# Kernel optimization log

Hardware: AMD Instinct MI355X
Metric: run time of the kernel (lower is better)

The kernel has to match this reference:

```python
import jax, jax.numpy as jnp
import numpy as np

NS, NR, D, H, O = 50000, 100000, 128, 128, 2
ESR, ERR, ESS = 1000000, 1600000, 800000


def _sage(x_src, x_dst, src, dst, Wl, bl, Wr, num_dst):
    # PyG SAGEConv(aggr='mean'): lin_l(mean_{j in N(i)} x_j) + lin_r(x_i)
    s = jax.ops.segment_sum(x_src[src], dst, num_segments=num_dst)
    cnt = jax.ops.segment_sum(jnp.ones(dst.shape, x_src.dtype), dst, num_segments=num_dst)
    agg = s / jnp.maximum(cnt, 1.0)[:, None]
    return agg @ Wl + bl + x_dst @ Wr


def setup_inputs() -> dict:
    key = jax.random.key(0)
    ks = jax.random.split(key, 32)
    f = lambda i, shp: jax.random.normal(ks[i], shp, jnp.float32) * 0.05
    inp = {"x_subject": f(0, (NS, D)), "x_roi": f(1, (NR, D))}
    wnames = ["w1_sr_l", "w1_sr_r", "w1_rr_l", "w1_rr_r", "w1_ss_l", "w1_ss_r",
              "w2_sr_l", "w2_sr_r", "w2_rr_l", "w2_rr_r", "w2_ss_l", "w2_ss_r"]
    for i, n in enumerate(wnames):
        inp[n] = f(2 + i, (D if n[1] == '1' else H, H))
    for n in ["b1_sr", "b1_rr", "b1_ss", "b2_sr", "b2_rr", "b2_ss"]:
        inp[n] = jnp.zeros((H,), jnp.float32)
    inp["lin_w"] = f(14, (H, O))
    inp["lin_b"] = jnp.zeros((O,), jnp.float32)
    inp["ei_sr_src"] = jax.random.randint(ks[20], (ESR,), 0, NS, jnp.int32)
    inp["ei_sr_dst"] = jax.random.randint(ks[21], (ESR,), 0, NR, jnp.int32)
    inp["ei_rr_src"] = jax.random.randint(ks[22], (ERR,), 0, NR, jnp.int32)
    inp["ei_rr_dst"] = jax.random.randint(ks[23], (ERR,), 0, NR, jnp.int32)
    inp["ei_ss_src"] = jax.random.randint(ks[24], (ESS,), 0, NS, jnp.int32)
    inp["ei_ss_dst"] = jax.random.randint(ks[25], (ESS,), 0, NS, jnp.int32)
    return inp


def reference(x_subject, x_roi,
              w1_sr_l, b1_sr, w1_sr_r, w1_rr_l, b1_rr, w1_rr_r, w1_ss_l, b1_ss, w1_ss_r,
              w2_sr_l, b2_sr, w2_sr_r, w2_rr_l, b2_rr, w2_rr_r, w2_ss_l, b2_ss, w2_ss_r,
              lin_w, lin_b,
              ei_sr_src, ei_sr_dst, ei_rr_src, ei_rr_dst, ei_ss_src, ei_ss_dst):
    # layer 1: HeteroConv with aggr='mean' over per-edge-type outputs
    r1 = 0.5 * (_sage(x_subject, x_roi, ei_sr_src, ei_sr_dst, w1_sr_l, b1_sr, w1_sr_r, NR)
                + _sage(x_roi, x_roi, ei_rr_src, ei_rr_dst, w1_rr_l, b1_rr, w1_rr_r, NR))
    s1 = _sage(x_subject, x_subject, ei_ss_src, ei_ss_dst, w1_ss_l, b1_ss, w1_ss_r, NS)
    r1, s1 = jax.nn.relu(r1), jax.nn.relu(s1)
    # layer 2 (roi branch is dead code w.r.t. the output, which reads only 'subject')
    s2 = _sage(s1, s1, ei_ss_src, ei_ss_dst, w2_ss_l, b2_ss, w2_ss_r, NS)
    s2 = jax.nn.relu(s2)
    return s2 @ lin_w + lin_b
```

## Files before the change

### kernel.cpp

```cpp
#include <hip/hip_runtime.h>

#define NS   50000
#define ESS  800000
#define D    128
#define SCAN_BLOCKS ((NS + 255) / 256)

typedef __attribute__((ext_vector_type(8))) short bf16x8;
typedef __attribute__((ext_vector_type(4))) float f32x4;

static __device__ __forceinline__ ushort f2bf(float f) {
    uint u = __float_as_uint(f);
    u += 0x7fffu + ((u >> 16) & 1u);
    return (ushort)(u >> 16);
}
static __device__ __forceinline__ float bf2f(ushort h) {
    return __uint_as_float((uint)h << 16);
}

__global__ __launch_bounds__(256) void split_x_k(
    const float* __restrict__ x, ushort* __restrict__ xh, int n8)
{
    int i = blockIdx.x * 256 + threadIdx.x;
    if (i >= n8) return;
    const float4* src = (const float4*)(x + (size_t)i * 8);
    float4 a = src[0], b = src[1];
    uint4 o;
    o.x = (uint)f2bf(a.x) | ((uint)f2bf(a.y) << 16);
    o.y = (uint)f2bf(a.z) | ((uint)f2bf(a.w) << 16);
    o.z = (uint)f2bf(b.x) | ((uint)f2bf(b.y) << 16);
    o.w = (uint)f2bf(b.z) | ((uint)f2bf(b.w) << 16);
    *(uint4*)(xh + (size_t)i * 8) = o;
}

__global__ __launch_bounds__(256) void prep_w_k(
    const float* __restrict__ w1l, const float* __restrict__ w1r,
    const float* __restrict__ w2l, const float* __restrict__ w2r,
    ushort* __restrict__ wt1h, ushort* __restrict__ wt1l,
    ushort* __restrict__ wt2h, ushort* __restrict__ wt2l)
{
    int t = blockIdx.x * 256 + threadIdx.x;
    int layer = t >> 15;
    int rem   = t & 32767;
    int k     = rem >> 7;
    int col   = rem & 127;
    const float* wl = layer ? w2l : w1l;
    const float* wr = layer ? w2r : w1r;
    float v = (k < 128) ? wl[k * 128 + col] : wr[(k - 128) * 128 + col];
    ushort h = f2bf(v);
    ushort l = f2bf(v - bf2f(h));
    size_t idx = ((size_t)((k >> 5) * 4 + ((k >> 3) & 3)) * 128 + col) * 8 + (k & 7);
    ushort* dh = layer ? wt2h : wt1h;
    ushort* dl = layer ? wt2l : wt1l;
    dh[idx] = h;
    dl[idx] = l;
}

__global__ __launch_bounds__(256) void count_deg_k(
    const int* __restrict__ dst, int* __restrict__ deg, int n)
{
    int e = blockIdx.x * 256 + threadIdx.x;
    if (e < n) atomicAdd(&deg[dst[e]], 1);
}

__global__ __launch_bounds__(256) void block_sum_k(
    const int* __restrict__ deg, int* __restrict__ bsum, int n)
{
    __shared__ int lds[256];
    int i = blockIdx.x * 256 + threadIdx.x;
    int v = (i < n) ? deg[i] : 0;
    lds[threadIdx.x] = v;
    __syncthreads();
    for (int off = 128; off > 0; off >>= 1) {
        if (threadIdx.x < off) lds[threadIdx.x] += lds[threadIdx.x + off];
        __syncthreads();
    }
    if (threadIdx.x == 0) bsum[blockIdx.x] = lds[0];
}

__global__ __launch_bounds__(256) void scan_partials_k(
    const int* __restrict__ bsum, int* __restrict__ boff, int nb)
{
    __shared__ int lds[256];
    int t = threadIdx.x;
    int v = (t < nb) ? bsum[t] : 0;
    lds[t] = v;
    __syncthreads();
    for (int off = 1; off < 256; off <<= 1) {
        int other = (t >= off) ? lds[t - off] : 0;
        __syncthreads();
        lds[t] += other;
        __syncthreads();
    }
    if (t < nb) boff[t] = lds[t] - v;
}

__global__ __launch_bounds__(256) void scan_final_k(
    const int* __restrict__ deg, const int* __restrict__ boff,
    int* __restrict__ row_start, int* __restrict__ pos, int n)
{
    __shared__ int lds[256];
    int t = threadIdx.x;
    int i = blockIdx.x * 256 + t;
    int v = (i < n) ? deg[i] : 0;
    lds[t] = v;
    __syncthreads();
    for (int off = 1; off < 256; off <<= 1) {
        int other = (t >= off) ? lds[t - off] : 0;
        __syncthreads();
        lds[t] += other;
        __syncthreads();
    }
    if (i < n) {
        int rs = boff[blockIdx.x] + lds[t] - v;
        row_start[i] = rs;
        pos[i] = rs;
    }
}

__global__ __launch_bounds__(256) void fill_csr_k(
    const int* __restrict__ src, const int* __restrict__ dst,
    int* __restrict__ pos, int* __restrict__ esrc, int n)
{
    int e = blockIdx.x * 256 + threadIdx.x;
    if (e < n) {
        int slot = atomicAdd(&pos[dst[e]], 1);
        esrc[slot] = src[e];
    }
}

__global__ __launch_bounds__(256) void gather_mean_bf16_k(
    const ushort* __restrict__ xh, const int* __restrict__ esrc,
    const int* __restrict__ row_start, const int* __restrict__ deg,
    ushort* __restrict__ aggh, ushort* __restrict__ aggl, int M)
{
    int d = blockIdx.x * 4 + (threadIdx.x >> 6);
    if (d >= M) return;
    int lane = threadIdx.x & 63;
    int beg = row_start[d];
    int n   = deg[d];
    const uint* xp = reinterpret_cast<const uint*>(xh);
    float a0x = 0.f, a0y = 0.f, a1x = 0.f, a1y = 0.f;
    float a2x = 0.f, a2y = 0.f, a3x = 0.f, a3y = 0.f;
    int j = 0;
    for (; j + 3 < n; j += 4) {
        int s0 = esrc[beg + j + 0];
        int s1 = esrc[beg + j + 1];
        int s2 = esrc[beg + j + 2];
        int s3 = esrc[beg + j + 3];
        uint u0 = xp[(size_t)s0 * 64 + lane];
        uint u1 = xp[(size_t)s1 * 64 + lane];
        uint u2 = xp[(size_t)s2 * 64 + lane];
        uint u3 = xp[(size_t)s3 * 64 + lane];
        a0x += __uint_as_float(u0 << 16); a0y += __uint_as_float(u0 & 0xffff0000u);
        a1x += __uint_as_float(u1 << 16); a1y += __uint_as_float(u1 & 0xffff0000u);
        a2x += __uint_as_float(u2 << 16); a2y += __uint_as_float(u2 & 0xffff0000u);
        a3x += __uint_as_float(u3 << 16); a3y += __uint_as_float(u3 & 0xffff0000u);
    }
    for (; j < n; ++j) {
        int s = esrc[beg + j];
        uint u = xp[(size_t)s * 64 + lane];
        a0x += __uint_as_float(u << 16); a0y += __uint_as_float(u & 0xffff0000u);
    }
    float ax = ((a0x + a1x) + (a2x + a3x));
    float ay = ((a0y + a1y) + (a2y + a3y));
    float scale = 1.0f / fmaxf((float)n, 1.0f);
    ax *= scale; ay *= scale;
    ushort hx = f2bf(ax), hy = f2bf(ay);
    ushort lx = f2bf(ax - bf2f(hx)), ly = f2bf(ay - bf2f(hy));
    reinterpret_cast<uint*>(aggh)[(size_t)d * 64 + lane] = (uint)hx | ((uint)hy << 16);
    reinterpret_cast<uint*>(aggl)[(size_t)d * 64 + lane] = (uint)lx | ((uint)ly << 16);
}

template<bool FINAL>
__global__ __launch_bounds__(256) void sage_mfma_k(
    const ushort* __restrict__ aggh, const ushort* __restrict__ aggl,
    const ushort* __restrict__ xh,
    const ushort* __restrict__ wth, const ushort* __restrict__ wtl,
    const float* __restrict__ bias,
    ushort* __restrict__ s_out,
    const float* __restrict__ lin_w, const float* __restrict__ lin_b,
    float* __restrict__ out, int M)
{
    __shared__ __align__(16) ushort Ah[4][64][8];
    __shared__ __align__(16) ushort Al[4][64][8];
    __shared__ __align__(16) ushort Bh[4][128][8];
    __shared__ __align__(16) ushort Bl[4][128][8];

    const int t    = threadIdx.x;
    const int rb   = blockIdx.x * 64;
    const int wid  = t >> 6;
    const int wm   = wid >> 1;
    const int wn   = wid & 1;
    const int lane = t & 63;
    const int lr   = lane & 15;
    const int kg   = lane >> 4;

    f32x4 acc[2][4] = {};

    for (int ks = 0; ks < 8; ++ks) {
        const bool isAgg = (ks < 4);
        {
            int row = t >> 2, kg2 = t & 3;
            int grow = rb + row;
            int kofs = (ks & 3) * 32 + kg2 * 8;
            uint4 vh = {0, 0, 0, 0}, vl = {0, 0, 0, 0};
            if (grow < M) {
                const ushort* ah = isAgg ? aggh : xh;
                vh = *(const uint4*)(ah + (size_t)grow * 128 + kofs);
                if (isAgg) vl = *(const uint4*)(aggl + (size_t)grow * 128 + kofs);
            }
            *(uint4*)&Ah[kg2][row][0] = vh;
            if (isAgg) *(uint4*)&Al[kg2][row][0] = vl;
        }
        {
            size_t base = (size_t)ks * 512;
            uint4* bhf = (uint4*)&Bh[0][0][0];
            uint4* blf = (uint4*)&Bl[0][0][0];
            const uint4* sh = (const uint4*)wth + base;
            const uint4* sl = (const uint4*)wtl + base;
            bhf[t * 2 + 0] = sh[t * 2 + 0];
            bhf[t * 2 + 1] = sh[t * 2 + 1];
            blf[t * 2 + 0] = sl[t * 2 + 0];
            blf[t * 2 + 1] = sl[t * 2 + 1];
        }
        __syncthreads();
        bf16x8 a_h[2], a_l[2], b_h[4], b_l[4];
        #pragma unroll
        for (int mt = 0; mt < 2; ++mt) {
            int r = wm * 32 + mt * 16 + lr;
            a_h[mt] = *(const bf16x8*)&Ah[kg][r][0];
            a_l[mt] = isAgg ? *(const bf16x8*)&Al[kg][r][0] : a_h[mt];
        }
        #pragma unroll
        for (int nt = 0; nt < 4; ++nt) {
            int c = wn * 64 + nt * 16 + lr;
            b_h[nt] = *(const bf16x8*)&Bh[kg][c][0];
            b_l[nt] = *(const bf16x8*)&Bl[kg][c][0];
        }
        #pragma unroll
        for (int mt = 0; mt < 2; ++mt) {
            #pragma unroll
            for (int nt = 0; nt < 4; ++nt) {
                acc[mt][nt] = __builtin_amdgcn_mfma_f32_16x16x32_bf16(
                    a_h[mt], b_h[nt], acc[mt][nt], 0, 0, 0);
                acc[mt][nt] = __builtin_amdgcn_mfma_f32_16x16x32_bf16(
                    a_h[mt], b_l[nt], acc[mt][nt], 0, 0, 0);
                if (isAgg)
                    acc[mt][nt] = __builtin_amdgcn_mfma_f32_16x16x32_bf16(
                        a_l[mt], b_h[nt], acc[mt][nt], 0, 0, 0);
            }
        }
        __syncthreads();
    }

    #pragma unroll
    for (int mt = 0; mt < 2; ++mt) {
        #pragma unroll
        for (int r = 0; r < 4; ++r) {
            int grow = rb + wm * 32 + mt * 16 + kg * 4 + r;
            if constexpr (FINAL) {
                float p0 = 0.f, p1 = 0.f;
                #pragma unroll
                for (int nt = 0; nt < 4; ++nt) {
                    int col = wn * 64 + nt * 16 + lr;
                    float v = fmaxf(acc[mt][nt][r] + bias[col], 0.f);
                    float2 lw = *(const float2*)(lin_w + col * 2);
                    p0 += v * lw.x;
                    p1 += v * lw.y;
                }
                #pragma unroll
                for (int off = 1; off < 16; off <<= 1) {
                    p0 += __shfl_xor(p0, off);
                    p1 += __shfl_xor(p1, off);
                }
                if (lr == 0 && grow < M) {
                    float b0 = (wn == 0) ? lin_b[0] : 0.f;
                    float b1 = (wn == 0) ? lin_b[1] : 0.f;
                    atomicAdd(&out[(size_t)grow * 2 + 0], p0 + b0);
                    atomicAdd(&out[(size_t)grow * 2 + 1], p1 + b1);
                }
            } else {
                #pragma unroll
                for (int nt = 0; nt < 4; ++nt) {
                    int col = wn * 64 + nt * 16 + lr;
                    float v = fmaxf(acc[mt][nt][r] + bias[col], 0.f);
                    if (grow < M)
                        s_out[(size_t)grow * 128 + col] = f2bf(v);
                }
            }
        }
    }
}

extern "C" void kernel_launch(void* const* d_in, const int* in_sizes, int n_in,
                              void* d_out, int out_size, void* d_ws, size_t ws_size,
                              hipStream_t stream)
{
    const float* x_subject = (const float*)d_in[0];
    const float* w1l  = (const float*)d_in[6];
    const float* w1r  = (const float*)d_in[7];
    const float* w2l  = (const float*)d_in[12];
    const float* w2r  = (const float*)d_in[13];
    const float* b1   = (const float*)d_in[16];
    const float* b2   = (const float*)d_in[19];
    const float* linw = (const float*)d_in[20];
    const float* linb = (const float*)d_in[21];
    const int* ss_src = (const int*)d_in[26];
    const int* ss_dst = (const int*)d_in[27];

    char* wp = (char*)d_ws;
    ushort* xh   = (ushort*)wp; wp += (size_t)NS * D * 2;
    ushort* s1h  = (ushort*)wp; wp += (size_t)NS * D * 2;
    ushort* aggh = (ushort*)wp; wp += (size_t)NS * D * 2;
    ushort* aggl = (ushort*)wp; wp += (size_t)NS * D * 2;
    ushort* wt1h = (ushort*)wp; wp += 256 * 128 * 2;
    ushort* wt1l = (ushort*)wp; wp += 256 * 128 * 2;
    ushort* wt2h = (ushort*)wp; wp += 256 * 128 * 2;
    ushort* wt2l = (ushort*)wp; wp += 256 * 128 * 2;
    int* deg       = (int*)wp; wp += NS * 4;
    int* row_start = (int*)wp; wp += NS * 4;
    int* pos       = (int*)wp; wp += NS * 4;
    int* esrc      = (int*)wp; wp += (size_t)ESS * 4;
    int* bsum      = (int*)wp; wp += SCAN_BLOCKS * 4;
    int* boff      = (int*)wp; wp += SCAN_BLOCKS * 4;

    const int edge_blocks = (ESS + 255) / 256;
    const int gath_blocks = (NS + 3) / 4;
    const int gemm_blocks = (NS + 63) / 64;

    hipMemsetAsync(deg, 0, NS * sizeof(int), stream);
    hipMemsetAsync(d_out, 0, (size_t)NS * 2 * sizeof(float), stream);

    split_x_k<<<(NS * D / 8 + 255) / 256, 256, 0, stream>>>(x_subject, xh, NS * D / 8);
    prep_w_k<<<256, 256, 0, stream>>>(w1l, w1r, w2l, w2r, wt1h, wt1l, wt2h, wt2l);

    count_deg_k<<<edge_blocks, 256, 0, stream>>>(ss_dst, deg, ESS);
    block_sum_k<<<SCAN_BLOCKS, 256, 0, stream>>>(deg, bsum, NS);
    scan_partials_k<<<1, 256, 0, stream>>>(bsum, boff, SCAN_BLOCKS);
    scan_final_k<<<SCAN_BLOCKS, 256, 0, stream>>>(deg, boff, row_start, pos, NS);
    fill_csr_k<<<edge_blocks, 256, 0, stream>>>(ss_src, ss_dst, pos, esrc, ESS);

    gather_mean_bf16_k<<<gath_blocks, 256, 0, stream>>>(xh, esrc, row_start,
                                                        deg, aggh, aggl, NS);
    sage_mfma_k<false><<<gemm_blocks, 256, 0, stream>>>(
        aggh, aggl, xh, wt1h, wt1l, b1, s1h, nullptr, nullptr, nullptr, NS);

    gather_mean_bf16_k<<<gath_blocks, 256, 0, stream>>>(s1h, esrc, row_start,
                                                        deg, aggh, aggl, NS);
    sage_mfma_k<true><<<gemm_blocks, 256, 0, stream>>>(
        aggh, aggl, s1h, wt2h, wt2l, b2, nullptr, linw, linb, (float*)d_out, NS);
}
```

Measured before the change: 358.7 us.

## Build CSR via two-level bucket sort; deepen gather unroll; stage full A tile in GEMM

Global-atomic degree counting and CSR fill are replaced with a two-pass bucket sort. Per-block LDS histograms over 256-node buckets are scanned, edges are scattered into a packed staging array, and each bucket is then sorted locally in LDS. This removes contended global atomics on scattered addresses. Separately, the gather loop issues 8 independent row loads per iteration instead of 4, and the GEMM loads the whole A tile into LDS once while reading weights straight from global memory, which removes the per-k-step barriers. The packing puts the source index into 16 bits, which assumes NS < 65536.

```diff
diff --git a/kernel.cpp b/kernel.cpp
--- a/kernel.cpp
+++ b/kernel.cpp
@@ -3,7 +3,13 @@
 #define NS   50000
 #define ESS  800000
 #define D    128
-#define SCAN_BLOCKS ((NS + 255) / 256)
+
+#define BSPAN 256
+#define NB    ((NS + BSPAN - 1) / BSPAN)
+#define EPB   4096
+#define NBLK  ((ESS + EPB - 1) / EPB)
+#define NHIST (NB * NBLK)
+#define SCAN2_BLOCKS ((NHIST + 255) / 256)
 
 typedef __attribute__((ext_vector_type(8))) short bf16x8;
 typedef __attribute__((ext_vector_type(4))) float f32x4;
@@ -55,11 +61,20 @@
     dl[idx] = l;
 }
 
-__global__ __launch_bounds__(256) void count_deg_k(
-    const int* __restrict__ dst, int* __restrict__ deg, int n)
-{
-    int e = blockIdx.x * 256 + threadIdx.x;
-    if (e < n) atomicAdd(&deg[dst[e]], 1);
+__global__ __launch_bounds__(256) void hist_k(
+    const int* __restrict__ dst, int* __restrict__ blockhist)
+{
+    __shared__ int lh[NB];
+    int t = threadIdx.x, blk = blockIdx.x;
+    if (t < NB) lh[t] = 0;
+    __syncthreads();
+    #pragma unroll
+    for (int i = 0; i < EPB / 256; ++i) {
+        int e = blk * EPB + i * 256 + t;
+        if (e < ESS) atomicAdd(&lh[dst[e] >> 8], 1);
+    }
+    __syncthreads();
+    if (t < NB) blockhist[t * NBLK + blk] = lh[t];
 }
 
 __global__ __launch_bounds__(256) void block_sum_k(
@@ -96,7 +111,7 @@
 
 __global__ __launch_bounds__(256) void scan_final_k(
     const int* __restrict__ deg, const int* __restrict__ boff,
-    int* __restrict__ row_start, int* __restrict__ pos, int n)
+    int* __restrict__ row_start, int n)
 {
     __shared__ int lds[256];
     int t = threadIdx.x;
@@ -110,21 +125,64 @@
         lds[t] += other;
         __syncthreads();
     }
-    if (i < n) {
-        int rs = boff[blockIdx.x] + lds[t] - v;
-        row_start[i] = rs;
-        pos[i] = rs;
-    }
-}
-
-__global__ __launch_bounds__(256) void fill_csr_k(
+    if (i < n) row_start[i] = boff[blockIdx.x] + lds[t] - v;
+}
+
+__global__ __launch_bounds__(256) void scatter_pairs_k(
     const int* __restrict__ src, const int* __restrict__ dst,
-    int* __restrict__ pos, int* __restrict__ esrc, int n)
-{
-    int e = blockIdx.x * 256 + threadIdx.x;
-    if (e < n) {
-        int slot = atomicAdd(&pos[dst[e]], 1);
-        esrc[slot] = src[e];
+    const int* __restrict__ shist, uint* __restrict__ staging)
+{
+    __shared__ int lcur[NB];
+    int t = threadIdx.x, blk = blockIdx.x;
+    if (t < NB) lcur[t] = shist[t * NBLK + blk];
+    __syncthreads();
+    #pragma unroll
+    for (int i = 0; i < EPB / 256; ++i) {
+        int e = blk * EPB + i * 256 + t;
+        if (e < ESS) {
+            int d = dst[e];
+            int slot = atomicAdd(&lcur[d >> 8], 1);
+            staging[slot] = (uint)src[e] | ((uint)(d & 255) << 16);
+        }
+    }
+}
+
+__global__ __launch_bounds__(256) void bucket_csr_k(
+    const uint* __restrict__ staging, const int* __restrict__ shist,
+    int* __restrict__ deg, int* __restrict__ row_start,
+    int* __restrict__ esrc)
+{
+    __shared__ int ldeg[BSPAN], lscan[BSPAN], lcur[BSPAN];
+    int b = blockIdx.x, t = threadIdx.x;
+    int base = shist[b * NBLK];
+    int next = (b == NB - 1) ? ESS : shist[(b + 1) * NBLK];
+    int n = next - base;
+    ldeg[t] = 0;
+    __syncthreads();
+    for (int i = t; i < n; i += 256)
+        atomicAdd(&ldeg[staging[base + i] >> 16], 1);
+    __syncthreads();
+    int v = ldeg[t];
+    lscan[t] = v;
+    __syncthreads();
+    for (int off = 1; off < 256; off <<= 1) {
+        int o = (t >= off) ? lscan[t - off] : 0;
+        __syncthreads();
+        lscan[t] += o;
+        __syncthreads();
+    }
+    int excl = lscan[t] - v;
+    int node = b * BSPAN + t;
+    if (node < NS) {
+        deg[node] = v;
+        row_start[node] = base + excl;
+    }
+    lcur[t] = base + excl;
+    __syncthreads();
+    for (int i = t; i < n; i += 256) {
+        uint p = staging[base + i];
+        int slot = atomicAdd(&lcur[p >> 16], 1);
+        esrc[slot] = (int)(p & 0xffffu);
     }
 }
 
@@ -139,30 +197,29 @@
     int beg = row_start[d];
     int n   = deg[d];
     const uint* xp = reinterpret_cast<const uint*>(xh);
-    float a0x = 0.f, a0y = 0.f, a1x = 0.f, a1y = 0.f;
-    float a2x = 0.f, a2y = 0.f, a3x = 0.f, a3y = 0.f;
+    float sx[8] = {}, sy[8] = {};
     int j = 0;
-    for (; j + 3 < n; j += 4) {
-        int s0 = esrc[beg + j + 0];
-        int s1 = esrc[beg + j + 1];
-        int s2 = esrc[beg + j + 2];
-        int s3 = esrc[beg + j + 3];
-        uint u0 = xp[(size_t)s0 * 64 + lane];
-        uint u1 = xp[(size_t)s1 * 64 + lane];
-        uint u2 = xp[(size_t)s2 * 64 + lane];
-        uint u3 = xp[(size_t)s3 * 64 + lane];
-        a0x += __uint_as_float(u0 << 16); a0y += __uint_as_float(u0 & 0xffff0000u);
-        a1x += __uint_as_float(u1 << 16); a1y += __uint_as_float(u1 & 0xffff0000u);
-        a2x += __uint_as_float(u2 << 16); a2y += __uint_as_float(u2 & 0xffff0000u);
-        a3x += __uint_as_float(u3 << 16); a3y += __uint_as_float(u3 & 0xffff0000u);
+    for (; j + 7 < n; j += 8) {
+        uint u[8];
+        #pragma unroll
+        for (int q = 0; q < 8; ++q) {
+            int s = esrc[beg + j + q];
+            u[q] = xp[(size_t)s * 64 + lane];
+        }
+        #pragma unroll
+        for (int q = 0; q < 8; ++q) {
+            sx[q] += __uint_as_float(u[q] << 16);
+            sy[q] += __uint_as_float(u[q] & 0xffff0000u);
+        }
     }
     for (; j < n; ++j) {
         int s = esrc[beg + j];
         uint u = xp[(size_t)s * 64 + lane];
-        a0x += __uint_as_float(u << 16); a0y += __uint_as_float(u & 0xffff0000u);
-    }
-    float ax = ((a0x + a1x) + (a2x + a3x));
-    float ay = ((a0y + a1y) + (a2y + a3y));
+        sx[0] += __uint_as_float(u << 16);
+        sy[0] += __uint_as_float(u & 0xffff0000u);
+    }
+    float ax = ((sx[0] + sx[1]) + (sx[2] + sx[3])) + ((sx[4] + sx[5]) + (sx[6] + sx[7]));
+    float ay = ((sy[0] + sy[1]) + (sy[2] + sy[3])) + ((sy[4] + sy[5]) + (sy[6] + sy[7]));
     float scale = 1.0f / fmaxf((float)n, 1.0f);
     ax *= scale; ay *= scale;
     ushort hx = f2bf(ax), hy = f2bf(ay);
@@ -181,10 +238,8 @@
     const float* __restrict__ lin_w, const float* __restrict__ lin_b,
     float* __restrict__ out, int M)
 {
-    __shared__ __align__(16) ushort Ah[4][64][8];
-    __shared__ __align__(16) ushort Al[4][64][8];
-    __shared__ __align__(16) ushort Bh[4][128][8];
-    __shared__ __align__(16) ushort Bl[4][128][8];
+    __shared__ __align__(16) ushort Ahs[8][4][64][8];
+    __shared__ __align__(16) ushort Als[4][4][64][8];
 
     const int t    = threadIdx.x;
     const int rb   = blockIdx.x * 64;
@@ -195,62 +250,60 @@
     const int lr   = lane & 15;
     const int kg   = lane >> 4;
 
+    {
+        int row = t >> 2, q = t & 3;
+        int grow = rb + row;
+        bool ok = grow < M;
+        #pragma unroll
+        for (int i = 0; i < 8; ++i) {
+            const ushort* sp = (i < 4)
+                ? aggh + (size_t)grow * 128 + i * 32 + q * 8
+                : xh   + (size_t)grow * 128 + (i - 4) * 32 + q * 8;
+            uint4 v = make_uint4(0, 0, 0, 0);
+            if (ok) v = *(const uint4*)sp;
+            *(uint4*)&Ahs[i][q][row][0] = v;
+        }
+        #pragma unroll
+        for (int i = 0; i < 4; ++i) {
+            const ushort* sp = aggl + (size_t)grow * 128 + i * 32 + q * 8;
+            uint4 v = make_uint4(0, 0, 0, 0);
+            if (ok) v = *(const uint4*)sp;
+            *(uint4*)&Als[i][q][row][0] = v;
+        }
+    }
+    __syncthreads();
+
     f32x4 acc[2][4] = {};
-
+    #pragma unroll
     for (int ks = 0; ks < 8; ++ks) {
         const bool isAgg = (ks < 4);
-        {
-            int row = t >> 2, kg2 = t & 3;
-            int grow = rb + row;
-            int kofs = (ks & 3) * 32 + kg2 * 8;
-            uint4 vh = {0, 0, 0, 0}, vl = {0, 0, 0, 0};
-            if (grow < M) {
-                const ushort* ah = isAgg ? aggh : xh;
-                vh = *(const uint4*)(ah + (size_t)grow * 128 + kofs);
-                if (isAgg) vl = *(const uint4*)(aggl + (size_t)grow * 128 + kofs);
-            }
-            *(uint4*)&Ah[kg2][row][0] = vh;
-            if (isAgg) *(uint4*)&Al[kg2][row][0] = vl;
-        }
-        {
-            size_t base = (size_t)ks * 512;
-            uint4* bhf = (uint4*)&Bh[0][0][0];
-            uint4* blf = (uint4*)&Bl[0][0][0];
-            const uint4* sh = (const uint4*)wth + base;
-            const uint4* sl = (const uint4*)wtl + base;
-            bhf[t * 2 + 0] = sh[t * 2 + 0];
-            bhf[t * 2 + 1] = sh[t * 2 + 1];
-            blf[t * 2 + 0] = sl[t * 2 + 0];
-            blf[t * 2 + 1] = sl[t * 2 + 1];
-        }
-        __syncthreads();
-        bf16x8 a_h[2], a_l[2], b_h[4], b_l[4];
+        bf16x8 ah[2], al[2], bh[4], bl[4];
+        #pragma unroll
+        for (int nt = 0; nt < 4; ++nt) {
+            int c = wn * 64 + nt * 16 + lr;
+            size_t off = ((size_t)(ks * 4 + kg) * 128 + c) * 8;
+            bh[nt] = *(const bf16x8*)(wth + off);
+            bl[nt] = *(const bf16x8*)(wtl + off);
+        }
         #pragma unroll
         for (int mt = 0; mt < 2; ++mt) {
             int r = wm * 32 + mt * 16 + lr;
-            a_h[mt] = *(const bf16x8*)&Ah[kg][r][0];
-            a_l[mt] = isAgg ? *(const bf16x8*)&Al[kg][r][0] : a_h[mt];
-        }
-        #pragma unroll
-        for (int nt = 0; nt < 4; ++nt) {
-            int c = wn * 64 + nt * 16 + lr;
-            b_h[nt] = *(const bf16x8*)&Bh[kg][c][0];
-            b_l[nt] = *(const bf16x8*)&Bl[kg][c][0];
+            ah[mt] = *(const bf16x8*)&Ahs[ks][kg][r][0];
+            al[mt] = isAgg ? *(const bf16x8*)&Als[ks][kg][r][0] : ah[mt];
         }
         #pragma unroll
         for (int mt = 0; mt < 2; ++mt) {
             #pragma unroll
             for (int nt = 0; nt < 4; ++nt) {
                 acc[mt][nt] = __builtin_amdgcn_mfma_f32_16x16x32_bf16(
-                    a_h[mt], b_h[nt], acc[mt][nt], 0, 0, 0);
+                    ah[mt], bh[nt], acc[mt][nt], 0, 0, 0);
                 acc[mt][nt] = __builtin_amdgcn_mfma_f32_16x16x32_bf16(
-                    a_h[mt], b_l[nt], acc[mt][nt], 0, 0, 0);
+                    ah[mt], bl[nt], acc[mt][nt], 0, 0, 0);
                 if (isAgg)
                     acc[mt][nt] = __builtin_amdgcn_mfma_f32_16x16x32_bf16(
-                        a_l[mt], b_h[nt], acc[mt][nt], 0, 0, 0);
+                        al[mt], bh[nt], acc[mt][nt], 0, 0, 0);
             }
         }
-        __syncthreads();
     }
 
     #pragma unroll
@@ -309,36 +362,37 @@
     const int* ss_dst = (const int*)d_in[27];
 
     char* wp = (char*)d_ws;
-    ushort* xh   = (ushort*)wp; wp += (size_t)NS * D * 2;
-    ushort* s1h  = (ushort*)wp; wp += (size_t)NS * D * 2;
-    ushort* aggh = (ushort*)wp; wp += (size_t)NS * D * 2;
-    ushort* aggl = (ushort*)wp; wp += (size_t)NS * D * 2;
-    ushort* wt1h = (ushort*)wp; wp += 256 * 128 * 2;
-    ushort* wt1l = (ushort*)wp; wp += 256 * 128 * 2;
-    ushort* wt2h = (ushort*)wp; wp += 256 * 128 * 2;
-    ushort* wt2l = (ushort*)wp; wp += 256 * 128 * 2;
-    int* deg       = (int*)wp; wp += NS * 4;
-    int* row_start = (int*)wp; wp += NS * 4;
-    int* pos       = (int*)wp; wp += NS * 4;
-    int* esrc      = (int*)wp; wp += (size_t)ESS * 4;
-    int* bsum      = (int*)wp; wp += SCAN_BLOCKS * 4;
-    int* boff      = (int*)wp; wp += SCAN_BLOCKS * 4;
-
-    const int edge_blocks = (ESS + 255) / 256;
+    ushort* xh      = (ushort*)wp; wp += (size_t)NS * D * 2;
+    ushort* s1h     = (ushort*)wp; wp += (size_t)NS * D * 2;
+    ushort* aggh    = (ushort*)wp; wp += (size_t)NS * D * 2;
+    ushort* aggl    = (ushort*)wp; wp += (size_t)NS * D * 2;
+    ushort* wt1h    = (ushort*)wp; wp += 256 * 128 * 2;
+    ushort* wt1l    = (ushort*)wp; wp += 256 * 128 * 2;
+    ushort* wt2h    = (ushort*)wp; wp += 256 * 128 * 2;
+    ushort* wt2l    = (ushort*)wp; wp += 256 * 128 * 2;
+    uint*  staging  = (uint*)wp;  wp += (size_t)ESS * 4;
+    int*   esrc     = (int*)wp;   wp += (size_t)ESS * 4;
+    int*   blockhist= (int*)wp;   wp += (size_t)NHIST * 4;
+    int*   shist    = (int*)wp;   wp += (size_t)NHIST * 4;
+    int*   deg      = (int*)wp;   wp += NS * 4;
+    int*   row_start= (int*)wp;   wp += NS * 4;
+    int*   bsum     = (int*)wp;   wp += 256 * 4;
+    int*   boff     = (int*)wp;   wp += 256 * 4;
+
     const int gath_blocks = (NS + 3) / 4;
     const int gemm_blocks = (NS + 63) / 64;
 
-    hipMemsetAsync(deg, 0, NS * sizeof(int), stream);
     hipMemsetAsync(d_out, 0, (size_t)NS * 2 * sizeof(float), stream);
 
     split_x_k<<<(NS * D / 8 + 255) / 256, 256, 0, stream>>>(x_subject, xh, NS * D / 8);
     prep_w_k<<<256, 256, 0, stream>>>(w1l, w1r, w2l, w2r, wt1h, wt1l, wt2h, wt2l);
 
-    count_deg_k<<<edge_blocks, 256, 0, stream>>>(ss_dst, deg, ESS);
-    block_sum_k<<<SCAN_BLOCKS, 256, 0, stream>>>(deg, bsum, NS);
-    scan_partials_k<<<1, 256, 0, stream>>>(bsum, boff, SCAN_BLOCKS);
-    scan_final_k<<<SCAN_BLOCKS, 256, 0, stream>>>(deg, boff, row_start, pos, NS);
-    fill_csr_k<<<edge_blocks, 256, 0, stream>>>(ss_src, ss_dst, pos, esrc, ESS);
+    hist_k<<<NBLK, 256, 0, stream>>>(ss_dst, blockhist);
+    block_sum_k<<<SCAN2_BLOCKS, 256, 0, stream>>>(blockhist, bsum, NHIST);
+    scan_partials_k<<<1, 256, 0, stream>>>(bsum, boff, SCAN2_BLOCKS);
+    scan_final_k<<<SCAN2_BLOCKS, 256, 0, stream>>>(blockhist, boff, shist, NHIST);
+    scatter_pairs_k<<<NBLK, 256, 0, stream>>>(ss_src, ss_dst, shist, staging);
+    bucket_csr_k<<<NB, 256, 0, stream>>>(staging, shist, deg, row_start, esrc);
 
     gather_mean_bf16_k<<<gath_blocks, 256, 0, stream>>>(xh, esrc, row_start,
                                                         deg, aggh, aggl, NS);
```

Measured after the change: 314.4 us. -12.3%, faster.
